# Kernel optimization log

Measured on AMD Instinct MI355X. Metric: run time of the kernel, lower is better.

Reference implementation:

```python
import jax, jax.numpy as jnp
import numpy as np

N = 50000
E = 800000
IN_CH = 128
HID = 64
HEADS = 4
G = 64  # number of graphs in batch
NEG_SLOPE = 0.2


def setup_inputs() -> dict:
    key = jax.random.key(0)
    ks = jax.random.split(key, 16)
    s = lambda fan_in: 1.0 / np.sqrt(fan_in)
    x = jax.random.normal(ks[0], (N, IN_CH), dtype=jnp.float32)
    edge_index = jax.random.randint(ks[1], (2, E), 0, N, dtype=jnp.int64)
    batch = jnp.sort(jax.random.randint(ks[2], (N,), 0, G, dtype=jnp.int64))
    # GAT layer 1: in 128 -> heads*hid = 256
    W1 = jax.random.uniform(ks[3], (IN_CH, HEADS * HID), jnp.float32, -s(IN_CH), s(IN_CH))
    a1_src = jax.random.uniform(ks[4], (HEADS, HID), jnp.float32, -s(HID), s(HID))
    a1_dst = jax.random.uniform(ks[5], (HEADS, HID), jnp.float32, -s(HID), s(HID))
    b1 = jnp.zeros((HEADS * HID,), jnp.float32)
    # GAT layer 2: in 256 -> heads*hid = 256
    W2 = jax.random.uniform(ks[6], (HEADS * HID, HEADS * HID), jnp.float32, -s(HEADS * HID), s(HEADS * HID))
    a2_src = jax.random.uniform(ks[7], (HEADS, HID), jnp.float32, -s(HID), s(HID))
    a2_dst = jax.random.uniform(ks[8], (HEADS, HID), jnp.float32, -s(HID), s(HID))
    b2 = jnp.zeros((HEADS * HID,), jnp.float32)
    # post-pool MLP: (in + 2*heads*hid) -> 256 -> 128
    d_cat = IN_CH + 2 * HEADS * HID
    W3 = jax.random.uniform(ks[9], (d_cat, 256), jnp.float32, -s(d_cat), s(d_cat))
    b3 = jnp.zeros((256,), jnp.float32)
    W4 = jax.random.uniform(ks[10], (256, 128), jnp.float32, -s(256), s(256))
    b4 = jnp.zeros((128,), jnp.float32)
    return {"x": x, "edge_index": edge_index, "batch": batch,
            "W1": W1, "a1_src": a1_src, "a1_dst": a1_dst, "b1": b1,
            "W2": W2, "a2_src": a2_src, "a2_dst": a2_dst, "b2": b2,
            "W3": W3, "b3": b3, "W4": W4, "b4": b4}


def gat_layer(x, src, dst, W, a_src, a_dst, b):
    n = x.shape[0]
    h = (x @ W).reshape(n, HEADS, HID)                 # [N,H,D]
    e_src = jnp.einsum('nhd,hd->nh', h, a_src)         # [N,H]
    e_dst = jnp.einsum('nhd,hd->nh', h, a_dst)
    e = jax.nn.leaky_relu(e_src[src] + e_dst[dst], NEG_SLOPE)  # [E,H]
    # segment softmax over incoming edges of each destination node
    m = jax.ops.segment_max(e, dst, num_segments=n)
    m = jnp.where(jnp.isfinite(m), m, 0.0)
    ex = jnp.exp(e - m[dst])
    denom = jax.ops.segment_sum(ex, dst, num_segments=n)
    alpha = ex / (denom[dst] + 1e-16)                  # [E,H]
    msg = h[src] * alpha[:, :, None]                   # [E,H,D]
    out = jax.ops.segment_sum(msg, dst, num_segments=n)
    return out.reshape(n, HEADS * HID) + b


def reference(x, edge_index, batch, W1, a1_src, a1_dst, b1, W2, a2_src, a2_dst, b2, W3, b3, W4, b4):
    src, dst = edge_index[0], edge_index[1]
    h0 = x
    h1 = jax.nn.relu(gat_layer(h0, src, dst, W1, a1_src, a1_dst, b1))
    h2 = jax.nn.relu(gat_layer(h1, src, dst, W2, a2_src, a2_dst, b2))
    comb = jnp.concatenate([h0, h1, h2], axis=-1)      # [N, 128+256+256]
    sums = jax.ops.segment_sum(comb, batch, num_segments=G)
    cnt = jax.ops.segment_sum(jnp.ones((x.shape[0],), comb.dtype), batch, num_segments=G)
    pooled = sums / jnp.maximum(cnt, 1.0)[:, None]     # [G, 640]
    hmlp = jax.nn.relu(pooled @ W3 + b3)               # dropout is identity at eval
    return hmlp @ W4 + b4                              # [G, 128]
```

## Files before the change

### kernel.cpp

```cpp
#include <hip/hip_runtime.h>
#include <cstdint>
#include <cstddef>

#define N_NODES 50000
#define E_EDGES 800000
#define INCH 128
#define HID 64
#define HEADS 4
#define NHD 256
#define NGRAPH 64
#define DCAT 640
#define NEG_SLOPE 0.2f

typedef __attribute__((ext_vector_type(8))) short bf16x8;
typedef __attribute__((ext_vector_type(4))) float f32x4;

static __device__ inline unsigned short f2bf(float f) {
    unsigned int u = __float_as_uint(f);
    unsigned int r = (u + 0x7FFFu + ((u >> 16) & 1u)) >> 16;
    return (unsigned short)r;
}
static __device__ inline float bf2f(unsigned short b) {
    return __uint_as_float(((unsigned int)b) << 16);
}

__global__ void wsplit_kernel(const float* __restrict__ W,
                              unsigned short* __restrict__ Wthi,
                              unsigned short* __restrict__ Wtlo, int K)
{
    const int i = blockIdx.x * 256 + threadIdx.x;
    if (i >= K * NHD) return;
    const int n = i / K, k = i - n * K;
    const float v = W[(size_t)k * NHD + n];
    const unsigned short hi = f2bf(v);
    Wthi[i] = hi;
    Wtlo[i] = f2bf(v - bf2f(hi));
}

#define GK 32
#define LDAB 40

__global__ __launch_bounds__(256, 2) void gemm_mfma(
    const float* __restrict__ A,
    const unsigned short* __restrict__ Bthi,
    const unsigned short* __restrict__ Btlo,
    const float* __restrict__ asrc, const float* __restrict__ adst,
    unsigned short* __restrict__ Cb, float* __restrict__ es,
    float* __restrict__ ed, int M, int K)
{
    __shared__ unsigned short Ahi[128 * LDAB];
    __shared__ unsigned short Alo[128 * LDAB];
    __shared__ unsigned short Bhi[128 * LDAB];
    __shared__ unsigned short Blo[128 * LDAB];

    const int t    = threadIdx.x;
    const int row0 = blockIdx.x * 128;
    const int col0 = blockIdx.y * 128;
    const int wave = t >> 6, lane = t & 63;
    const int wr = (wave >> 1) * 64;
    const int wc = (wave & 1) * 64;
    const int m16 = lane & 15, quad = lane >> 4;

    f32x4 acc[4][4];
#pragma unroll
    for (int i = 0; i < 4; ++i)
#pragma unroll
        for (int j = 0; j < 4; ++j) acc[i][j] = (f32x4){0.f, 0.f, 0.f, 0.f};

    for (int k0 = 0; k0 < K; k0 += GK) {
#pragma unroll
        for (int i = 0; i < 4; ++i) {
            const int seg = t + i * 256;
            const int r = seg >> 3, p = seg & 7;
            const int grow = row0 + r;
            float4 v = make_float4(0.f, 0.f, 0.f, 0.f);
            if (grow < M) v = *(const float4*)(A + (size_t)grow * K + k0 + p * 4);
            ushort4 hv, lv;
            hv.x = f2bf(v.x); lv.x = f2bf(v.x - bf2f(hv.x));
            hv.y = f2bf(v.y); lv.y = f2bf(v.y - bf2f(hv.y));
            hv.z = f2bf(v.z); lv.z = f2bf(v.z - bf2f(hv.z));
            hv.w = f2bf(v.w); lv.w = f2bf(v.w - bf2f(hv.w));
            *(ushort4*)(&Ahi[r * LDAB + p * 4]) = hv;
            *(ushort4*)(&Alo[r * LDAB + p * 4]) = lv;
        }
#pragma unroll
        for (int i = 0; i < 2; ++i) {
            const int seg = t + i * 256;
            const int r = seg >> 2, p = seg & 3;
            const size_t goff = (size_t)(col0 + r) * K + k0 + p * 8;
            *(int4*)(&Bhi[r * LDAB + p * 8]) = *(const int4*)(Bthi + goff);
            *(int4*)(&Blo[r * LDAB + p * 8]) = *(const int4*)(Btlo + goff);
        }
        __syncthreads();

        bf16x8 afh[4], afl[4], bfh[4], bfl[4];
#pragma unroll
        for (int i = 0; i < 4; ++i) {
            const int r = wr + i * 16 + m16;
            afh[i] = *(const bf16x8*)(&Ahi[r * LDAB + quad * 8]);
            afl[i] = *(const bf16x8*)(&Alo[r * LDAB + quad * 8]);
        }
#pragma unroll
        for (int j = 0; j < 4; ++j) {
            const int n = wc + j * 16 + m16;
            bfh[j] = *(const bf16x8*)(&Bhi[n * LDAB + quad * 8]);
            bfl[j] = *(const bf16x8*)(&Blo[n * LDAB + quad * 8]);
        }
#pragma unroll
        for (int i = 0; i < 4; ++i)
#pragma unroll
            for (int j = 0; j < 4; ++j) {
                acc[i][j] = __builtin_amdgcn_mfma_f32_16x16x32_bf16(afh[i], bfh[j], acc[i][j], 0, 0, 0);
                acc[i][j] = __builtin_amdgcn_mfma_f32_16x16x32_bf16(afh[i], bfl[j], acc[i][j], 0, 0, 0);
                acc[i][j] = __builtin_amdgcn_mfma_f32_16x16x32_bf16(afl[i], bfh[j], acc[i][j], 0, 0, 0);
            }
        __syncthreads();
    }

#pragma unroll
    for (int i = 0; i < 4; ++i)
#pragma unroll
        for (int reg = 0; reg < 4; ++reg) {
            const int r = row0 + wr + i * 16 + quad * 4 + reg;
            if (r < M) {
#pragma unroll
                for (int j = 0; j < 4; ++j)
                    Cb[(size_t)r * NHD + col0 + wc + j * 16 + m16] = f2bf(acc[i][j][reg]);
            }
        }

    const int head = (col0 + wc) >> 6;
    float a_s[4], a_d[4];
#pragma unroll
    for (int j = 0; j < 4; ++j) {
        a_s[j] = asrc[head * HID + j * 16 + m16];
        a_d[j] = adst[head * HID + j * 16 + m16];
    }
#pragma unroll
    for (int i = 0; i < 4; ++i)
#pragma unroll
        for (int reg = 0; reg < 4; ++reg) {
            float ps = 0.f, pd = 0.f;
#pragma unroll
            for (int j = 0; j < 4; ++j) {
                const float v = acc[i][j][reg];
                ps += v * a_s[j];
                pd += v * a_d[j];
            }
#pragma unroll
            for (int off = 1; off < 16; off <<= 1) {
                ps += __shfl_xor(ps, off, 64);
                pd += __shfl_xor(pd, off, 64);
            }
            if (m16 == 0) {
                const int r = row0 + wr + i * 16 + quad * 4 + reg;
                if (r < M) {
                    es[r * HEADS + head] = ps;
                    ed[r * HEADS + head] = pd;
                }
            }
        }
}

__global__ void hist_kernel(const int* __restrict__ ei, int* __restrict__ counts)
{
    const int e = blockIdx.x * 256 + threadIdx.x;
    if (e >= E_EDGES) return;
    atomicAdd(&counts[ei[E_EDGES + e]], 1);
}

#define SBLK 1024
#define NSCB ((N_NODES + SBLK - 1) / SBLK)

__global__ __launch_bounds__(1024) void scan_local_kernel(
    const int* __restrict__ counts, int* __restrict__ offsets,
    int* __restrict__ bsum)
{
    __shared__ int tmp[SBLK];
    const int t = threadIdx.x;
    const int i = blockIdx.x * SBLK + t;
    const int v = (i < N_NODES) ? counts[i] : 0;
    tmp[t] = v;
    __syncthreads();
    for (int off = 1; off < SBLK; off <<= 1) {
        const int u = (t >= off) ? tmp[t - off] : 0;
        __syncthreads();
        tmp[t] += u;
        __syncthreads();
    }
    if (i < N_NODES) offsets[i] = tmp[t] - v;
    if (t == SBLK - 1) bsum[blockIdx.x] = tmp[t];
}

__global__ __launch_bounds__(1024) void scan_final_kernel(
    int* __restrict__ offsets, int* __restrict__ cursor,
    const int* __restrict__ bsum)
{
    __shared__ int base_sh;
    const int b = blockIdx.x;
    if (threadIdx.x == 0) {
        int s = 0;
        for (int j = 0; j < b; ++j) s += bsum[j];
        base_sh = s;
    }
    __syncthreads();
    const int i = b * SBLK + threadIdx.x;
    if (i < N_NODES) {
        const int v = offsets[i] + base_sh;
        offsets[i] = v;
        cursor[i]  = v;
    }
    if (b == 0 && threadIdx.x == 0) offsets[N_NODES] = E_EDGES;
}

__global__ void scatter_kernel(const int* __restrict__ ei, int* __restrict__ cursor,
                               int* __restrict__ csr)
{
    const int e = blockIdx.x * 256 + threadIdx.x;
    if (e >= E_EDGES) return;
    const int d = ei[E_EDGES + e];
    const int pos = atomicAdd(&cursor[d], 1);
    csr[pos] = e;
}

__global__ __launch_bounds__(256) void aggregate_fused(
    const unsigned short* __restrict__ hb, const int* __restrict__ ei,
    const int* __restrict__ csr, const int* __restrict__ offsets,
    const float* __restrict__ es, const float* __restrict__ ed,
    const float* __restrict__ bias, float* __restrict__ out,
    unsigned short* __restrict__ outb)
{
    const int wid  = threadIdx.x >> 6;
    const int lane = threadIdx.x & 63;
    const int node = blockIdx.x * 4 + wid;
    if (node >= N_NODES) return;
    const int head = lane >> 4;
    const int col  = lane * 4;
    const int sub  = lane & 15;

    const float edc = ed[node * 4 + head];
    const int beg = offsets[node], end = offsets[node + 1];

    float4 acc = make_float4(0.f, 0.f, 0.f, 0.f);
    float dsum = 0.f;

    int base = beg;
    int m_cur = min(16, end - base);
    int s_cur = 0; float w_cur = 0.f;
    if (base < end && sub < m_cur) {
        const int eid = csr[base + sub];
        s_cur = ei[eid];
        float u = es[s_cur * 4 + head] + edc;
        u = u > 0.f ? u : NEG_SLOPE * u;
        w_cur = expf(u);
    }

    while (base < end) {
        const int base_n = base + 16;
        const int m_nxt = min(16, end - base_n);
        int s_nxt = 0; float w_nxt = 0.f;
        if (base_n < end && sub < m_nxt) {
            const int eid = csr[base_n + sub];
            s_nxt = ei[eid];
            float u = es[s_nxt * 4 + head] + edc;
            u = u > 0.f ? u : NEG_SLOPE * u;
            w_nxt = expf(u);
        }
        if (m_cur == 16) {
#pragma unroll
            for (int i = 0; i < 16; ++i) {
                const int   s = (int)__builtin_amdgcn_readlane((unsigned)s_cur, i);
                const float w = __shfl(w_cur, (lane & 48) + i, 64);
                const ushort4 v = *(const ushort4*)(hb + (size_t)s * NHD + col);
                acc.x += w * bf2f(v.x);
                acc.y += w * bf2f(v.y);
                acc.z += w * bf2f(v.z);
                acc.w += w * bf2f(v.w);
                dsum += w;
            }
        } else {
            for (int i = 0; i < m_cur; ++i) {
                const int   s = __shfl(s_cur, i, 64);
                const float w = __shfl(w_cur, (lane & 48) + i, 64);
                const ushort4 v = *(const ushort4*)(hb + (size_t)s * NHD + col);
                acc.x += w * bf2f(v.x);
                acc.y += w * bf2f(v.y);
                acc.z += w * bf2f(v.z);
                acc.w += w * bf2f(v.w);
                dsum += w;
            }
        }
        s_cur = s_nxt; w_cur = w_nxt; m_cur = m_nxt; base = base_n;
    }

    const float inv = 1.0f / (dsum + 1e-16f);
    const float4 bb = *(const float4*)(bias + col);
    float4 o;
    o.x = fmaxf(acc.x * inv + bb.x, 0.f);
    o.y = fmaxf(acc.y * inv + bb.y, 0.f);
    o.z = fmaxf(acc.z * inv + bb.z, 0.f);
    o.w = fmaxf(acc.w * inv + bb.w, 0.f);
    if (out) *(float4*)(out + (size_t)node * NHD + col) = o;
    ushort4 ob;
    ob.x = f2bf(o.x); ob.y = f2bf(o.y); ob.z = f2bf(o.z); ob.w = f2bf(o.w);
    *(ushort4*)(outb + (size_t)node * NHD + col) = ob;
}

__global__ void graph_offsets_kernel(const int* __restrict__ batch, int* __restrict__ goff)
{
    const int n = blockIdx.x * 256 + threadIdx.x;
    if (n >= N_NODES) return;
    const int b  = batch[n];
    const int bp = (n == 0) ? -1 : batch[n - 1];
    for (int g = bp + 1; g <= b; ++g) goff[g] = n;
    if (n == N_NODES - 1) {
        for (int g = b + 1; g <= NGRAPH; ++g) goff[g] = N_NODES;
    }
}

#define PRB 128

__global__ __launch_bounds__(640) void pool_sum_kernel(
    const float* __restrict__ x, const unsigned short* __restrict__ h1b,
    const unsigned short* __restrict__ h2b, const int* __restrict__ batch,
    float* __restrict__ sums)
{
    __shared__ int bsh[PRB];
    const int c  = threadIdx.x;
    const int r0 = blockIdx.x * PRB;
    const int r1 = min(N_NODES, r0 + PRB);
    const int nr = r1 - r0;
    if (c < nr) bsh[c] = batch[r0 + c];
    __syncthreads();

    const float* srcf = nullptr;
    const unsigned short* srcb = nullptr;
    int ld, cc;
    if (c < INCH)            { srcf = x;   ld = INCH; cc = c; }
    else if (c < INCH + NHD) { srcb = h1b; ld = NHD;  cc = c - INCH; }
    else                     { srcb = h2b; ld = NHD;  cc = c - INCH - NHD; }

    float sum = 0.f;
    int g = bsh[0];
    for (int i = 0; i < nr; ++i) {
        const int gb = bsh[i];
        if (gb != g) {
            atomicAdd(&sums[g * DCAT + c], sum);
            sum = 0.f;
            g = gb;
        }
        sum += srcf ? srcf[(size_t)(r0 + i) * ld + cc]
                    : bf2f(srcb[(size_t)(r0 + i) * ld + cc]);
    }
    atomicAdd(&sums[g * DCAT + c], sum);
}

__global__ void pool_finalize_kernel(const float* __restrict__ sums,
                                     const int* __restrict__ goff,
                                     float* __restrict__ pooled)
{
    const int i = blockIdx.x * 256 + threadIdx.x;
    if (i >= NGRAPH * DCAT) return;
    const int g = i / DCAT;
    const float cnt = (float)(goff[g + 1] - goff[g]);
    pooled[i] = sums[i] / fmaxf(cnt, 1.0f);
}

__global__ __launch_bounds__(256) void mlp_kernel(
    const float* __restrict__ pooled, const float* __restrict__ W3,
    const float* __restrict__ b3, const float* __restrict__ W4,
    const float* __restrict__ b4, float* __restrict__ out)
{
    const int g = blockIdx.x;
    __shared__ float p[DCAT];
    __shared__ float hm[256];
    for (int i = threadIdx.x; i < DCAT; i += 256) p[i] = pooled[(size_t)g * DCAT + i];
    __syncthreads();
    float s = b3[threadIdx.x];
    for (int k = 0; k < DCAT; ++k) s += p[k] * W3[(size_t)k * 256 + threadIdx.x];
    hm[threadIdx.x] = fmaxf(s, 0.f);
    __syncthreads();
    if (threadIdx.x < 128) {
        float o = b4[threadIdx.x];
        for (int k = 0; k < 256; ++k) o += hm[k] * W4[(size_t)k * 128 + threadIdx.x];
        out[(size_t)g * 128 + threadIdx.x] = o;
    }
}

extern "C" void kernel_launch(void* const* d_in, const int* in_sizes, int n_in,
                              void* d_out, int out_size, void* d_ws, size_t ws_size,
                              hipStream_t stream)
{
    const float* x     = (const float*)d_in[0];
    const int*   ei    = (const int*)d_in[1];
    const int*   batch = (const int*)d_in[2];
    const float* W1    = (const float*)d_in[3];
    const float* a1s   = (const float*)d_in[4];
    const float* a1d   = (const float*)d_in[5];
    const float* b1    = (const float*)d_in[6];
    const float* W2    = (const float*)d_in[7];
    const float* a2s   = (const float*)d_in[8];
    const float* a2d   = (const float*)d_in[9];
    const float* b2    = (const float*)d_in[10];
    const float* W3    = (const float*)d_in[11];
    const float* b3    = (const float*)d_in[12];
    const float* W4    = (const float*)d_in[13];
    const float* b4    = (const float*)d_in[14];
    float* out = (float*)d_out;

    size_t off = 0;
    auto carve = [&](size_t bytes) -> void* {
        void* p = (char*)d_ws + off;
        off = (off + bytes + 255) & ~(size_t)255;
        return p;
    };
    unsigned short* hrawb = (unsigned short*)carve((size_t)N_NODES * NHD * 2);
    float*          h1    = (float*)carve((size_t)N_NODES * NHD * 4);
    unsigned short* h1b   = (unsigned short*)carve((size_t)N_NODES * NHD * 2);
    unsigned short* h2b   = (unsigned short*)carve((size_t)N_NODES * NHD * 2);
    float* es     = (float*)carve((size_t)N_NODES * HEADS * 4);
    float* ed     = (float*)carve((size_t)N_NODES * HEADS * 4);
    float* pooled = (float*)carve((size_t)NGRAPH * DCAT * 4);
    float* psums  = (float*)carve((size_t)NGRAPH * DCAT * 4);
    int*   counts  = (int*)carve((size_t)N_NODES * 4);
    int*   offsets = (int*)carve((size_t)(N_NODES + 1) * 4);
    int*   cursor  = (int*)carve((size_t)N_NODES * 4);
    int*   csr     = (int*)carve((size_t)E_EDGES * 4);
    int*   goff    = (int*)carve((size_t)(NGRAPH + 1) * 4);
    int*   bsum    = (int*)carve((size_t)NSCB * 4);
    unsigned short* w1thi = (unsigned short*)carve((size_t)NHD * INCH * 2);
    unsigned short* w1tlo = (unsigned short*)carve((size_t)NHD * INCH * 2);
    unsigned short* w2thi = (unsigned short*)carve((size_t)NHD * NHD * 2);
    unsigned short* w2tlo = (unsigned short*)carve((size_t)NHD * NHD * 2);

    const int egrid = (E_EDGES + 255) / 256;
    const int ngrid = (N_NODES + 255) / 256;

    hipMemsetAsync(counts, 0, (size_t)N_NODES * 4, stream);
    hist_kernel<<<egrid, 256, 0, stream>>>(ei, counts);
    scan_local_kernel<<<NSCB, SBLK, 0, stream>>>(counts, offsets, bsum);
    scan_final_kernel<<<NSCB, SBLK, 0, stream>>>(offsets, cursor, bsum);
    scatter_kernel<<<egrid, 256, 0, stream>>>(ei, cursor, csr);
    graph_offsets_kernel<<<ngrid, 256, 0, stream>>>(batch, goff);
    wsplit_kernel<<<(INCH * NHD + 255) / 256, 256, 0, stream>>>(W1, w1thi, w1tlo, INCH);
    wsplit_kernel<<<(NHD * NHD + 255) / 256, 256, 0, stream>>>(W2, w2thi, w2tlo, NHD);

    dim3 ggrid((N_NODES + 127) / 128, NHD / 128);

    gemm_mfma<<<ggrid, 256, 0, stream>>>(x, w1thi, w1tlo, a1s, a1d,
                                         hrawb, es, ed, N_NODES, INCH);
    aggregate_fused<<<(N_NODES + 3) / 4, 256, 0, stream>>>(hrawb, ei, csr, offsets,
                                                           es, ed, b1, h1, h1b);
    gemm_mfma<<<ggrid, 256, 0, stream>>>(h1, w2thi, w2tlo, a2s, a2d,
                                         hrawb, es, ed, N_NODES, NHD);
    aggregate_fused<<<(N_NODES + 3) / 4, 256, 0, stream>>>(hrawb, ei, csr, offsets,
                                                           es, ed, b2, nullptr, h2b);

    hipMemsetAsync(psums, 0, (size_t)NGRAPH * DCAT * 4, stream);
    pool_sum_kernel<<<(N_NODES + PRB - 1) / PRB, 640, 0, stream>>>(x, h1b, h2b, batch, psums);
    pool_finalize_kernel<<<(NGRAPH * DCAT + 255) / 256, 256, 0, stream>>>(psums, goff, pooled);
    mlp_kernel<<<NGRAPH, 256, 0, stream>>>(pooled, W3, b3, W4, b4, out);
}
```

Baseline: 506.5 us.

## Pre-split GEMM A operands into bf16 hi/lo and raise K tile to 64

```diff
diff --git a/kernel.cpp b/kernel.cpp
--- a/kernel.cpp
+++ b/kernel.cpp
@@ -3,6 +3,7 @@
 #include <cstddef>
 
 #define N_NODES 50000
+#define M_PAD 50048
 #define E_EDGES 800000
 #define INCH 128
 #define HID 64
@@ -37,11 +38,24 @@
     Wtlo[i] = f2bf(v - bf2f(hi));
 }
 
-#define GK 32
-#define LDAB 40
+__global__ void asplit_kernel(const float* __restrict__ A,
+                              unsigned short* __restrict__ Ahi,
+                              unsigned short* __restrict__ Alo, int n)
+{
+    const int i = blockIdx.x * 256 + threadIdx.x;
+    if (i >= n) return;
+    const float v = A[i];
+    const unsigned short h = f2bf(v);
+    Ahi[i] = h;
+    Alo[i] = f2bf(v - bf2f(h));
+}
+
+#define GK 64
+#define LDAB 72
 
 __global__ __launch_bounds__(256, 2) void gemm_mfma(
-    const float* __restrict__ A,
+    const unsigned short* __restrict__ Athi,
+    const unsigned short* __restrict__ Atlo,
     const unsigned short* __restrict__ Bthi,
     const unsigned short* __restrict__ Btlo,
     const float* __restrict__ asrc, const float* __restrict__ adst,
@@ -71,49 +85,40 @@
 #pragma unroll
         for (int i = 0; i < 4; ++i) {
             const int seg = t + i * 256;
-            const int r = seg >> 3, p = seg & 7;
-            const int grow = row0 + r;
-            float4 v = make_float4(0.f, 0.f, 0.f, 0.f);
-            if (grow < M) v = *(const float4*)(A + (size_t)grow * K + k0 + p * 4);
-            ushort4 hv, lv;
-            hv.x = f2bf(v.x); lv.x = f2bf(v.x - bf2f(hv.x));
-            hv.y = f2bf(v.y); lv.y = f2bf(v.y - bf2f(hv.y));
-            hv.z = f2bf(v.z); lv.z = f2bf(v.z - bf2f(hv.z));
-            hv.w = f2bf(v.w); lv.w = f2bf(v.w - bf2f(hv.w));
-            *(ushort4*)(&Ahi[r * LDAB + p * 4]) = hv;
-            *(ushort4*)(&Alo[r * LDAB + p * 4]) = lv;
-        }
-#pragma unroll
-        for (int i = 0; i < 2; ++i) {
-            const int seg = t + i * 256;
-            const int r = seg >> 2, p = seg & 3;
-            const size_t goff = (size_t)(col0 + r) * K + k0 + p * 8;
-            *(int4*)(&Bhi[r * LDAB + p * 8]) = *(const int4*)(Bthi + goff);
-            *(int4*)(&Blo[r * LDAB + p * 8]) = *(const int4*)(Btlo + goff);
+            const int r = seg >> 3, p = (seg & 7) * 8;
+            const size_t ga = (size_t)(row0 + r) * K + k0 + p;
+            const size_t gb = (size_t)(col0 + r) * K + k0 + p;
+            *(int4*)(&Ahi[r * LDAB + p]) = *(const int4*)(Athi + ga);
+            *(int4*)(&Alo[r * LDAB + p]) = *(const int4*)(Atlo + ga);
+            *(int4*)(&Bhi[r * LDAB + p]) = *(const int4*)(Bthi + gb);
+            *(int4*)(&Blo[r * LDAB + p]) = *(const int4*)(Btlo + gb);
         }
         __syncthreads();
 
-        bf16x8 afh[4], afl[4], bfh[4], bfl[4];
-#pragma unroll
-        for (int i = 0; i < 4; ++i) {
-            const int r = wr + i * 16 + m16;
-            afh[i] = *(const bf16x8*)(&Ahi[r * LDAB + quad * 8]);
-            afl[i] = *(const bf16x8*)(&Alo[r * LDAB + quad * 8]);
-        }
-#pragma unroll
-        for (int j = 0; j < 4; ++j) {
-            const int n = wc + j * 16 + m16;
-            bfh[j] = *(const bf16x8*)(&Bhi[n * LDAB + quad * 8]);
-            bfl[j] = *(const bf16x8*)(&Blo[n * LDAB + quad * 8]);
-        }
-#pragma unroll
-        for (int i = 0; i < 4; ++i)
+#pragma unroll
+        for (int h = 0; h < 2; ++h) {
+            bf16x8 afh[4], afl[4], bfh[4], bfl[4];
+#pragma unroll
+            for (int i = 0; i < 4; ++i) {
+                const int r = wr + i * 16 + m16;
+                afh[i] = *(const bf16x8*)(&Ahi[r * LDAB + h * 32 + quad * 8]);
+                afl[i] = *(const bf16x8*)(&Alo[r * LDAB + h * 32 + quad * 8]);
+            }
 #pragma unroll
             for (int j = 0; j < 4; ++j) {
-                acc[i][j] = __builtin_amdgcn_mfma_f32_16x16x32_bf16(afh[i], bfh[j], acc[i][j], 0, 0, 0);
-                acc[i][j] = __builtin_amdgcn_mfma_f32_16x16x32_bf16(afh[i], bfl[j], acc[i][j], 0, 0, 0);
-                acc[i][j] = __builtin_amdgcn_mfma_f32_16x16x32_bf16(afl[i], bfh[j], acc[i][j], 0, 0, 0);
-            }
+                const int n = wc + j * 16 + m16;
+                bfh[j] = *(const bf16x8*)(&Bhi[n * LDAB + h * 32 + quad * 8]);
+                bfl[j] = *(const bf16x8*)(&Blo[n * LDAB + h * 32 + quad * 8]);
+            }
+#pragma unroll
+            for (int i = 0; i < 4; ++i)
+#pragma unroll
+                for (int j = 0; j < 4; ++j) {
+                    acc[i][j] = __builtin_amdgcn_mfma_f32_16x16x32_bf16(afh[i], bfh[j], acc[i][j], 0, 0, 0);
+                    acc[i][j] = __builtin_amdgcn_mfma_f32_16x16x32_bf16(afh[i], bfl[j], acc[i][j], 0, 0, 0);
+                    acc[i][j] = __builtin_amdgcn_mfma_f32_16x16x32_bf16(afl[i], bfh[j], acc[i][j], 0, 0, 0);
+                }
+        }
         __syncthreads();
     }
 
@@ -227,8 +232,8 @@
     const unsigned short* __restrict__ hb, const int* __restrict__ ei,
     const int* __restrict__ csr, const int* __restrict__ offsets,
     const float* __restrict__ es, const float* __restrict__ ed,
-    const float* __restrict__ bias, float* __restrict__ out,
-    unsigned short* __restrict__ outb)
+    const float* __restrict__ bias, unsigned short* __restrict__ outhi,
+    unsigned short* __restrict__ outlo)
 {
     const int wid  = threadIdx.x >> 6;
     const int lane = threadIdx.x & 63;
@@ -300,10 +305,17 @@
     o.y = fmaxf(acc.y * inv + bb.y, 0.f);
     o.z = fmaxf(acc.z * inv + bb.z, 0.f);
     o.w = fmaxf(acc.w * inv + bb.w, 0.f);
-    if (out) *(float4*)(out + (size_t)node * NHD + col) = o;
-    ushort4 ob;
-    ob.x = f2bf(o.x); ob.y = f2bf(o.y); ob.z = f2bf(o.z); ob.w = f2bf(o.w);
-    *(ushort4*)(outb + (size_t)node * NHD + col) = ob;
+    ushort4 oh;
+    oh.x = f2bf(o.x); oh.y = f2bf(o.y); oh.z = f2bf(o.z); oh.w = f2bf(o.w);
+    *(ushort4*)(outhi + (size_t)node * NHD + col) = oh;
+    if (outlo) {
+        ushort4 ol;
+        ol.x = f2bf(o.x - bf2f(oh.x));
+        ol.y = f2bf(o.y - bf2f(oh.y));
+        ol.z = f2bf(o.z - bf2f(oh.z));
+        ol.w = f2bf(o.w - bf2f(oh.w));
+        *(ushort4*)(outlo + (size_t)node * NHD + col) = ol;
+    }
 }
 
 __global__ void graph_offsets_kernel(const int* __restrict__ batch, int* __restrict__ goff)
@@ -414,10 +426,12 @@
         off = (off + bytes + 255) & ~(size_t)255;
         return p;
     };
-    unsigned short* hrawb = (unsigned short*)carve((size_t)N_NODES * NHD * 2);
-    float*          h1    = (float*)carve((size_t)N_NODES * NHD * 4);
-    unsigned short* h1b   = (unsigned short*)carve((size_t)N_NODES * NHD * 2);
-    unsigned short* h2b   = (unsigned short*)carve((size_t)N_NODES * NHD * 2);
+    unsigned short* xhi   = (unsigned short*)carve((size_t)M_PAD * INCH * 2);
+    unsigned short* xlo   = (unsigned short*)carve((size_t)M_PAD * INCH * 2);
+    unsigned short* ghi   = (unsigned short*)carve((size_t)N_NODES * NHD * 2);
+    unsigned short* h1hi  = (unsigned short*)carve((size_t)M_PAD * NHD * 2);
+    unsigned short* h1lo  = (unsigned short*)carve((size_t)M_PAD * NHD * 2);
+    unsigned short* h2hi  = (unsigned short*)carve((size_t)N_NODES * NHD * 2);
     float* es     = (float*)carve((size_t)N_NODES * HEADS * 4);
     float* ed     = (float*)carve((size_t)N_NODES * HEADS * 4);
     float* pooled = (float*)carve((size_t)NGRAPH * DCAT * 4);
@@ -444,20 +458,21 @@
     graph_offsets_kernel<<<ngrid, 256, 0, stream>>>(batch, goff);
     wsplit_kernel<<<(INCH * NHD + 255) / 256, 256, 0, stream>>>(W1, w1thi, w1tlo, INCH);
     wsplit_kernel<<<(NHD * NHD + 255) / 256, 256, 0, stream>>>(W2, w2thi, w2tlo, NHD);
-
-    dim3 ggrid((N_NODES + 127) / 128, NHD / 128);
-
-    gemm_mfma<<<ggrid, 256, 0, stream>>>(x, w1thi, w1tlo, a1s, a1d,
-                                         hrawb, es, ed, N_NODES, INCH);
-    aggregate_fused<<<(N_NODES + 3) / 4, 256, 0, stream>>>(hrawb, ei, csr, offsets,
-                                                           es, ed, b1, h1, h1b);
-    gemm_mfma<<<ggrid, 256, 0, stream>>>(h1, w2thi, w2tlo, a2s, a2d,
-                                         hrawb, es, ed, N_NODES, NHD);
-    aggregate_fused<<<(N_NODES + 3) / 4, 256, 0, stream>>>(hrawb, ei, csr, offsets,
-                                                           es, ed, b2, nullptr, h2b);
+    asplit_kernel<<<(N_NODES * INCH + 255) / 256, 256, 0, stream>>>(x, xhi, xlo, N_NODES * INCH);
+
+    dim3 ggrid((M_PAD + 127) / 128, NHD / 128);
+
+    gemm_mfma<<<ggrid, 256, 0, stream>>>(xhi, xlo, w1thi, w1tlo, a1s, a1d,
+                                         ghi, es, ed, N_NODES, INCH);
+    aggregate_fused<<<(N_NODES + 3) / 4, 256, 0, stream>>>(ghi, ei, csr, offsets,
+                                                           es, ed, b1, h1hi, h1lo);
+    gemm_mfma<<<ggrid, 256, 0, stream>>>(h1hi, h1lo, w2thi, w2tlo, a2s, a2d,
+                                         ghi, es, ed, N_NODES, NHD);
+    aggregate_fused<<<(N_NODES + 3) / 4, 256, 0, stream>>>(ghi, ei, csr, offsets,
+                                                           es, ed, b2, h2hi, nullptr);
 
     hipMemsetAsync(psums, 0, (size_t)NGRAPH * DCAT * 4, stream);
-    pool_sum_kernel<<<(N_NODES + PRB - 1) / PRB, 640, 0, stream>>>(x, h1b, h2b, batch, psums);
+    pool_sum_kernel<<<(N_NODES + PRB - 1) / PRB, 640, 0, stream>>>(x, h1hi, h2hi, batch, psums);
     pool_finalize_kernel<<<(NGRAPH * DCAT + 255) / 256, 256, 0, stream>>>(psums, goff, pooled);
     mlp_kernel<<<NGRAPH, 256, 0, stream>>>(pooled, W3, b3, W4, b4, out);
 }
```

Result: no change. 504.0 us (-0.5%).
